# Kernel optimization log

Measured on AMD Instinct MI355X. Metric: run time of the kernel, lower is better.

The kernel has to match this reference:

```python
import jax, jax.numpy as jnp
import numpy as np


def _wn(v, g):
    # weight-norm: w[o, i] = g[o] * v[o, i] / ||v[o, :]||
    return g[:, None] * v / jnp.linalg.norm(v, axis=1, keepdims=True)


def setup_inputs() -> dict:
    key = jax.random.key(0)
    ks = jax.random.split(key, 8)
    B, C, H, W = 16, 512, 64, 64
    K, D = 2048, 64
    return {
        "z": jax.random.normal(ks[0], (B, C, H, W), dtype=jnp.float32),
        "codebook": jax.random.normal(ks[1], (K, D), dtype=jnp.float32),
        "in_v": jax.random.normal(ks[2], (D, C), dtype=jnp.float32),
        "in_g": jax.random.uniform(ks[3], (D,), dtype=jnp.float32, minval=0.5, maxval=1.5),
        "in_b": jax.random.normal(ks[4], (D,), dtype=jnp.float32) * 0.02,
        "out_v": jax.random.normal(ks[5], (C, D), dtype=jnp.float32),
        "out_g": jax.random.uniform(ks[6], (C,), dtype=jnp.float32, minval=0.5, maxval=1.5),
        "out_b": jax.random.normal(ks[7], (C,), dtype=jnp.float32) * 0.02,
    }


def reference(z, codebook, in_v, in_g, in_b, out_v, out_g, out_b):
    COMMIT_W = 0.25
    B, C, H, W = z.shape
    D = codebook.shape[1]

    Wi = _wn(in_v, in_g)    # [D, C]
    Wo = _wn(out_v, out_g)  # [C, D]

    # in_proj (1x1 conv): b c h w -> b d h w
    z_e = jnp.einsum('bchw,dc->bdhw', z, Wi) + in_b[None, :, None, None]

    # flatten tokens: (b h w) d
    z_e_flat = z_e.transpose(0, 2, 3, 1).reshape(-1, D)

    dist = (jnp.sum(z_e_flat * z_e_flat, axis=1, keepdims=True)
            - 2.0 * z_e_flat @ codebook.T
            + jnp.sum(codebook * codebook, axis=1)[None, :])
    indices_flat = jnp.argmin(dist, axis=1)            # [(BHW)]
    indices = indices_flat.reshape(B, H, W)

    z_q_flat = codebook[indices_flat]                  # gather [(BHW), D]
    z_q = z_q_flat.reshape(B, H, W, D).transpose(0, 3, 1, 2)  # b d h w

    sg = jax.lax.stop_gradient
    commitment_loss = jnp.mean((sg(z_e) - z_q) ** 2)
    codebook_loss = jnp.mean((sg(z_q) - z_e) ** 2)
    vq_loss = codebook_loss + COMMIT_W * commitment_loss

    # straight-through
    z_q_st = z_e + sg(z_q - z_e)

    # out_proj (1x1 conv): b d h w -> b c h w
    out = jnp.einsum('bdhw,cd->bchw', z_q_st, Wo) + out_b[None, :, None, None]
    return out, indices, vq_loss
```

## Files before the change

kernel.cpp:

```cpp
#include <hip/hip_runtime.h>
#include <math.h>

#define TOK_PER_BLK 128


__global__ void k_prep_wi(const float* __restrict__ v, const float* __restrict__ g,
                          float* __restrict__ wi){
  const int d = blockIdx.x;
  const int tid = threadIdx.x;
  float s = 0.f;
  for (int c = tid; c < 512; c += 256){ float x = v[d*512+c]; s = fmaf(x,x,s); }
  __shared__ float red[4];
  #pragma unroll
  for (int o = 32; o > 0; o >>= 1) s += __shfl_down(s, o);
  if ((tid & 63) == 0) red[tid >> 6] = s;
  __syncthreads();
  const float nrm = sqrtf(red[0]+red[1]+red[2]+red[3]);
  const float gd = g[d];
  for (int c = tid; c < 512; c += 256) wi[d*512+c] = gd * v[d*512+c] / nrm;
}

__global__ void k_prep_wo(const float* __restrict__ v, const float* __restrict__ g,
                          float* __restrict__ wot){
  const int c = blockIdx.x;
  const int d = threadIdx.x;
  const float x = v[c*64+d];
  float s = x*x;
  #pragma unroll
  for (int o = 32; o > 0; o >>= 1) s += __shfl_down(s, o);
  const float nrm = __shfl(sqrtf(s), 0);
  wot[d*512 + c] = g[c] * x / nrm;
}

__global__ void k_table(const float* __restrict__ cbk, const float* __restrict__ wot,
                        const float* __restrict__ ob, float* __restrict__ table,
                        float* __restrict__ ne){
  const int k = blockIdx.x;
  const int tid = threadIdx.x;
  __shared__ float e[64];
  if (tid < 64) e[tid] = cbk[k*64 + tid];
  __syncthreads();
  if (tid < 64){
    float x = e[tid];
    float s = x*x;
    #pragma unroll
    for (int o = 32; o > 0; o >>= 1) s += __shfl_down(s, o);
    if (tid == 0) ne[k] = s;
  }
  const int c = tid;
  float acc = ob[c];
  #pragma unroll 16
  for (int d = 0; d < 64; d++) acc = fmaf(e[d], wot[d*512 + c], acc);
  table[(size_t)k*512 + c] = acc;
}

__global__ __launch_bounds__(256, 2) void k_main(
    const float* __restrict__ z, const float* __restrict__ cbk,
    const float* __restrict__ wi, const float* __restrict__ inb,
    const float* __restrict__ ne, const float* __restrict__ table,
    float* __restrict__ out, float* __restrict__ oidx, double* __restrict__ loss)
{
  __shared__ __align__(16) float ze_s[64*132];
  __shared__ __align__(16) float sbuf[64*132];
  __shared__ int bidx_s[128];

  const int tid = threadIdx.x;
  const int t0  = blockIdx.x * TOK_PER_BLK;
  const int b   = t0 >> 12;
  const int hw0 = t0 & 4095;
  const float* zb = z + ((size_t)b << 21) + hw0;

  float* z_s  = sbuf;
  float* wi_s = sbuf + 32*132;
  float acc1[4][8];
  #pragma unroll
  for (int j = 0; j < 4; j++)
    #pragma unroll
    for (int i = 0; i < 8; i++) acc1[j][i] = 0.f;

  const int tt = tid & 31;
  const int dg = tid >> 5;

  for (int c0 = 0; c0 < 512; c0 += 32){
    {
      const int cc = tid >> 3, colb = (tid & 7) * 16;
      const float* src = zb + (size_t)(c0 + cc) * 4096 + colb;
      float* dst = &z_s[cc*132 + colb];
      #pragma unroll
      for (int j = 0; j < 4; j++)
        *(float4*)(dst + 4*j) = *(const float4*)(src + 4*j);
    }
    {
      #pragma unroll
      for (int j = 0; j < 8; j++){
        const int flat = tid + 256*j;
        const int d = flat >> 5, cc = flat & 31;
        wi_s[cc*68 + d] = wi[d*512 + c0 + cc];
      }
    }
    __syncthreads();
    #pragma unroll 4
    for (int cc = 0; cc < 32; cc++){
      const float4 zv = *(const float4*)&z_s[cc*132 + tt*4];
      const float4 wa = *(const float4*)&wi_s[cc*68 + dg*8];
      const float4 wb = *(const float4*)&wi_s[cc*68 + dg*8 + 4];
      const float zzv[4] = {zv.x, zv.y, zv.z, zv.w};
      const float wwv[8] = {wa.x, wa.y, wa.z, wa.w, wb.x, wb.y, wb.z, wb.w};
      #pragma unroll
      for (int j = 0; j < 4; j++)
        #pragma unroll
        for (int i = 0; i < 8; i++)
          acc1[j][i] = fmaf(zzv[j], wwv[i], acc1[j][i]);
    }
    __syncthreads();
  }
  #pragma unroll
  for (int i = 0; i < 8; i++){
    const int d = dg*8 + i;
    const float bd = inb[d];
    #pragma unroll
    for (int j = 0; j < 4; j++)
      ze_s[d*132 + tt*4 + j] = acc1[j][i] + bd;
  }
  __syncthreads();

  float* cb_s = sbuf;
  const int tg = tid & 15;
  const int kg = tid >> 4;
  float best[8]; int bidx[8];
  #pragma unroll
  for (int j = 0; j < 8; j++){ best[j] = INFINITY; bidx[j] = 0; }

  for (int kc = 0; kc < 2048; kc += 128){
    #pragma unroll
    for (int j = 0; j < 32; j++){
      const int flat = tid + 256*j;
      const int kk = flat >> 6, d = flat & 63;
      cb_s[d*132 + kk] = -2.0f * cbk[(size_t)(kc + kk)*64 + d];
    }
    __syncthreads();
    float acc[8][8];
    #pragma unroll
    for (int i = 0; i < 8; i++){
      const float nv = ne[kc + kg*8 + i];
      #pragma unroll
      for (int j = 0; j < 8; j++) acc[j][i] = nv;
    }
    #pragma unroll 4
    for (int d = 0; d < 64; d++){
      const float4 za  = *(const float4*)&ze_s[d*132 + tg*8];
      const float4 zb4 = *(const float4*)&ze_s[d*132 + tg*8 + 4];
      const float4 ca  = *(const float4*)&cb_s[d*132 + kg*8];
      const float4 cb4 = *(const float4*)&cb_s[d*132 + kg*8 + 4];
      const float zzv[8] = {za.x, za.y, za.z, za.w, zb4.x, zb4.y, zb4.z, zb4.w};
      const float ccv[8] = {ca.x, ca.y, ca.z, ca.w, cb4.x, cb4.y, cb4.z, cb4.w};
      #pragma unroll
      for (int j = 0; j < 8; j++)
        #pragma unroll
        for (int i = 0; i < 8; i++)
          acc[j][i] = fmaf(zzv[j], ccv[i], acc[j][i]);
    }
    #pragma unroll
    for (int i = 0; i < 8; i++){
      const int k = kc + kg*8 + i;
      #pragma unroll
      for (int j = 0; j < 8; j++)
        if (acc[j][i] < best[j]){ best[j] = acc[j][i]; bidx[j] = k; }
    }
    __syncthreads();
  }

  float* rb = sbuf;
  int*   ri = (int*)(sbuf + 2048);
  #pragma unroll
  for (int j = 0; j < 8; j++){
    const int t = tg*8 + j;
    rb[t*16 + kg] = best[j];
    ri[t*16 + kg] = bidx[j];
  }
  __syncthreads();

  float myloss = 0.f;
  if (tid < 128){
    const int t = tid;
    float bv = rb[t*16]; int bi = ri[t*16];
    #pragma unroll
    for (int q = 1; q < 16; q++){
      const float vq = rb[t*16 + q]; const int iq = ri[t*16 + q];
      if (vq < bv || (vq == bv && iq < bi)){ bv = vq; bi = iq; }
    }
    bidx_s[t] = bi;
    oidx[t0 + t] = (float)bi;
    const float* e = cbk + (size_t)bi * 64;
    #pragma unroll 8
    for (int d = 0; d < 64; d++){
      const float diff = ze_s[d*132 + t] - e[d];
      myloss = fmaf(diff, diff, myloss);
    }
  }
  #pragma unroll
  for (int o = 32; o > 0; o >>= 1) myloss += __shfl_down(myloss, o);
  if (tid < 128 && (tid & 63) == 0) atomicAdd(loss, (double)myloss);
  __syncthreads();

  {
    const int tl = tid & 127, cg = tid >> 7;
    const int myk = bidx_s[tl];
    const float* trow = table + ((size_t)myk << 9) + cg*256;
    float* ob = out + (((size_t)b) << 21) + hw0 + tl;
    #pragma unroll 4
    for (int ci = 0; ci < 64; ci++){
      const float4 v = *(const float4*)(trow + ci*4);
      const size_t cbase = (size_t)(cg*256 + ci*4) << 12;
      ob[cbase        ] = v.x;
      ob[cbase +  4096] = v.y;
      ob[cbase +  8192] = v.z;
      ob[cbase + 12288] = v.w;
    }
  }
}

__global__ void k_finish(const double* __restrict__ loss, float* __restrict__ oloss){
  *oloss = (float)(1.25 * (*loss) / 4194304.0);
}


extern "C" void kernel_launch(void* const* d_in, const int* in_sizes, int n_in,
                              void* d_out, int out_size, void* d_ws, size_t ws_size,
                              hipStream_t stream) {
  const float* z   = (const float*)d_in[0];
  const float* cbk = (const float*)d_in[1];
  const float* inv = (const float*)d_in[2];
  const float* ing = (const float*)d_in[3];
  const float* inb = (const float*)d_in[4];
  const float* ov  = (const float*)d_in[5];
  const float* og  = (const float*)d_in[6];
  const float* ob  = (const float*)d_in[7];

  float* ws    = (float*)d_ws;
  float* wi    = ws;
  float* wot   = ws + 32768;
  float* table = ws + 65536;
  float* ne    = ws + 65536 + 1048576;
  double* loss = (double*)(ws + 65536 + 1048576 + 2048);

  float* out   = (float*)d_out;
  float* oidx  = out + 33554432;
  float* oloss = out + 33619968;

  hipMemsetAsync(loss, 0, sizeof(double), stream);
  k_prep_wi<<<64, 256, 0, stream>>>(inv, ing, wi);
  k_prep_wo<<<512, 64, 0, stream>>>(ov, og, wot);
  k_table<<<2048, 512, 0, stream>>>(cbk, wot, ob, table, ne);
  k_main<<<512, 256, 0, stream>>>(z, cbk, wi, inb, ne, table, out, oidx, loss);
  k_finish<<<1, 1, 0, stream>>>(loss, oloss);
}
```

Before: 376.0 us.

## Split in-projection into separate kernel and retile codebook search with prefetch

Moves the 1x1 in-projection into its own kernel that computes 256 tokens per block with register-prefetched double buffering and a transposed Wi. It writes z_e to a workspace buffer. The VQ search kernel then reloads z_e and uses a larger 8x16 register tile, streaming the codebook in 256-entry, half-D chunks with register prefetch. This aims to raise arithmetic intensity and overlap loads, at the cost of an extra global round trip for z_e and an extra launch.

```diff
diff --git a/kernel.cpp b/kernel.cpp
--- a/kernel.cpp
+++ b/kernel.cpp
@@ -1,11 +1,10 @@
 #include <hip/hip_runtime.h>
 #include <math.h>
 
-#define TOK_PER_BLK 128
 
 
 __global__ void k_prep_wi(const float* __restrict__ v, const float* __restrict__ g,
-                          float* __restrict__ wi){
+                          float* __restrict__ wiT){
   const int d = blockIdx.x;
   const int tid = threadIdx.x;
   float s = 0.f;
@@ -17,7 +16,7 @@
   __syncthreads();
   const float nrm = sqrtf(red[0]+red[1]+red[2]+red[3]);
   const float gd = g[d];
-  for (int c = tid; c < 512; c += 256) wi[d*512+c] = gd * v[d*512+c] / nrm;
+  for (int c = tid; c < 512; c += 256) wiT[c*64 + d] = gd * v[d*512+c] / nrm;
 }
 
 __global__ void k_prep_wo(const float* __restrict__ v, const float* __restrict__ g,
@@ -54,127 +53,187 @@
   table[(size_t)k*512 + c] = acc;
 }
 
-__global__ __launch_bounds__(256, 2) void k_main(
-    const float* __restrict__ z, const float* __restrict__ cbk,
-    const float* __restrict__ wi, const float* __restrict__ inb,
+__global__ __launch_bounds__(256, 1) void k_inproj(
+    const float* __restrict__ z, const float* __restrict__ wiT,
+    const float* __restrict__ inb, float* __restrict__ ze)
+{
+  __shared__ __align__(16) float z_s[16*256];
+  __shared__ __align__(16) float wi_s[16*68];
+  const int tid = threadIdx.x;
+  const int T0  = blockIdx.x << 8;
+  const int b   = T0 >> 12;
+  const int hw0 = T0 & 4095;
+  const float* zb = z + ((size_t)b << 21) + hw0;
+
+  const int tgp = tid & 31;
+  const int dgp = tid >> 5;
+  const int ccb = tid >> 6;
+  const int c64 = tid & 63;
+
+  float acc[8][8];
+  #pragma unroll
+  for (int i = 0; i < 8; i++)
+    #pragma unroll
+    for (int j = 0; j < 8; j++) acc[i][j] = 0.f;
+
+  float4 pz[4]; float pw[4];
+  #pragma unroll
+  for (int q = 0; q < 4; q++){
+    pz[q] = *(const float4*)(zb + (size_t)(ccb + 4*q) * 4096 + c64*4);
+    pw[q] = wiT[(ccb + 4*q)*64 + c64];
+  }
+  #pragma unroll
+  for (int q = 0; q < 4; q++){
+    *(float4*)&z_s[(ccb + 4*q)*256 + c64*4] = pz[q];
+    wi_s[(ccb + 4*q)*68 + c64] = pw[q];
+  }
+  __syncthreads();
+
+  for (int c0 = 0;;){
+    const int nxt = c0 + 16;
+    if (nxt < 512){
+      #pragma unroll
+      for (int q = 0; q < 4; q++){
+        pz[q] = *(const float4*)(zb + (size_t)(nxt + ccb + 4*q) * 4096 + c64*4);
+        pw[q] = wiT[(nxt + ccb + 4*q)*64 + c64];
+      }
+    }
+    #pragma unroll 4
+    for (int cc = 0; cc < 16; cc++){
+      const float4 ta = *(const float4*)&z_s[cc*256 + tgp*4];
+      const float4 tb = *(const float4*)&z_s[cc*256 + 128 + tgp*4];
+      const float4 w0 = *(const float4*)&wi_s[cc*68 + dgp*8];
+      const float4 w1 = *(const float4*)&wi_s[cc*68 + dgp*8 + 4];
+      const float tv[8] = {ta.x,ta.y,ta.z,ta.w, tb.x,tb.y,tb.z,tb.w};
+      const float wv[8] = {w0.x,w0.y,w0.z,w0.w, w1.x,w1.y,w1.z,w1.w};
+      #pragma unroll
+      for (int i = 0; i < 8; i++)
+        #pragma unroll
+        for (int j = 0; j < 8; j++)
+          acc[i][j] = fmaf(tv[j], wv[i], acc[i][j]);
+    }
+    if (nxt >= 512) break;
+    __syncthreads();
+    #pragma unroll
+    for (int q = 0; q < 4; q++){
+      *(float4*)&z_s[(ccb + 4*q)*256 + c64*4] = pz[q];
+      wi_s[(ccb + 4*q)*68 + c64] = pw[q];
+    }
+    __syncthreads();
+    c0 = nxt;
+  }
+
+  #pragma unroll
+  for (int i = 0; i < 8; i++){
+    const int d = dgp*8 + i;
+    const float bd = inb[d];
+    float4 o0 = {acc[i][0]+bd, acc[i][1]+bd, acc[i][2]+bd, acc[i][3]+bd};
+    float4 o1 = {acc[i][4]+bd, acc[i][5]+bd, acc[i][6]+bd, acc[i][7]+bd};
+    *(float4*)(ze + (size_t)d*65536 + T0 + tgp*4)       = o0;
+    *(float4*)(ze + (size_t)d*65536 + T0 + 128 + tgp*4) = o1;
+  }
+}
+
+__global__ __launch_bounds__(256, 2) void k_main2(
+    const float* __restrict__ ze, const float* __restrict__ cbk,
     const float* __restrict__ ne, const float* __restrict__ table,
     float* __restrict__ out, float* __restrict__ oidx, double* __restrict__ loss)
 {
-  __shared__ __align__(16) float ze_s[64*132];
-  __shared__ __align__(16) float sbuf[64*132];
+  __shared__ __align__(16) float ze_s[64*128];
+  __shared__ __align__(16) float cb_s[32*260];
   __shared__ int bidx_s[128];
 
   const int tid = threadIdx.x;
-  const int t0  = blockIdx.x * TOK_PER_BLK;
+  const int t0  = blockIdx.x << 7;
   const int b   = t0 >> 12;
   const int hw0 = t0 & 4095;
-  const float* zb = z + ((size_t)b << 21) + hw0;
-
-  float* z_s  = sbuf;
-  float* wi_s = sbuf + 32*132;
-  float acc1[4][8];
-  #pragma unroll
-  for (int j = 0; j < 4; j++)
-    #pragma unroll
-    for (int i = 0; i < 8; i++) acc1[j][i] = 0.f;
-
-  const int tt = tid & 31;
-  const int dg = tid >> 5;
-
-  for (int c0 = 0; c0 < 512; c0 += 32){
-    {
-      const int cc = tid >> 3, colb = (tid & 7) * 16;
-      const float* src = zb + (size_t)(c0 + cc) * 4096 + colb;
-      float* dst = &z_s[cc*132 + colb];
-      #pragma unroll
-      for (int j = 0; j < 4; j++)
-        *(float4*)(dst + 4*j) = *(const float4*)(src + 4*j);
-    }
-    {
-      #pragma unroll
-      for (int j = 0; j < 8; j++){
-        const int flat = tid + 256*j;
-        const int d = flat >> 5, cc = flat & 31;
-        wi_s[cc*68 + d] = wi[d*512 + c0 + cc];
-      }
-    }
-    __syncthreads();
-    #pragma unroll 4
-    for (int cc = 0; cc < 32; cc++){
-      const float4 zv = *(const float4*)&z_s[cc*132 + tt*4];
-      const float4 wa = *(const float4*)&wi_s[cc*68 + dg*8];
-      const float4 wb = *(const float4*)&wi_s[cc*68 + dg*8 + 4];
-      const float zzv[4] = {zv.x, zv.y, zv.z, zv.w};
-      const float wwv[8] = {wa.x, wa.y, wa.z, wa.w, wb.x, wb.y, wb.z, wb.w};
-      #pragma unroll
-      for (int j = 0; j < 4; j++)
-        #pragma unroll
-        for (int i = 0; i < 8; i++)
-          acc1[j][i] = fmaf(zzv[j], wwv[i], acc1[j][i]);
-    }
-    __syncthreads();
-  }
-  #pragma unroll
-  for (int i = 0; i < 8; i++){
-    const int d = dg*8 + i;
-    const float bd = inb[d];
-    #pragma unroll
-    for (int j = 0; j < 4; j++)
-      ze_s[d*132 + tt*4 + j] = acc1[j][i] + bd;
-  }
-  __syncthreads();
-
-  float* cb_s = sbuf;
+
+  #pragma unroll
+  for (int j = 0; j < 8; j++){
+    const int idx = tid + 256*j;
+    const int row = idx >> 5, col4 = idx & 31;
+    *(float4*)&ze_s[row*128 + col4*4] =
+        *(const float4*)(ze + (size_t)row*65536 + t0 + col4*4);
+  }
+
   const int tg = tid & 15;
   const int kg = tid >> 4;
   float best[8]; int bidx[8];
   #pragma unroll
   for (int j = 0; j < 8; j++){ best[j] = INFINITY; bidx[j] = 0; }
 
-  for (int kc = 0; kc < 2048; kc += 128){
-    #pragma unroll
-    for (int j = 0; j < 32; j++){
-      const int flat = tid + 256*j;
-      const int kk = flat >> 6, d = flat & 63;
-      cb_s[d*132 + kk] = -2.0f * cbk[(size_t)(kc + kk)*64 + d];
-    }
+  float acc[8][16];
+  float4 pv[8];
+  {
+    const float* src = cbk + (size_t)tid * 64;
+    #pragma unroll
+    for (int q = 0; q < 8; q++) pv[q] = *(const float4*)(src + q*4);
+  }
+
+  for (int s = 0; s < 16; s++){
     __syncthreads();
-    float acc[8][8];
-    #pragma unroll
-    for (int i = 0; i < 8; i++){
-      const float nv = ne[kc + kg*8 + i];
-      #pragma unroll
-      for (int j = 0; j < 8; j++) acc[j][i] = nv;
-    }
+    #pragma unroll
+    for (int q = 0; q < 8; q++){
+      const float* p = (const float*)&pv[q];
+      #pragma unroll
+      for (int r = 0; r < 4; r++) cb_s[(q*4+r)*260 + tid] = -2.0f * p[r];
+    }
+    if (s < 15){
+      const int s1 = s + 1;
+      const float* src = cbk + (size_t)(((s1 >> 1) << 8) + tid) * 64 + (s1 & 1)*32;
+      #pragma unroll
+      for (int q = 0; q < 8; q++) pv[q] = *(const float4*)(src + q*4);
+    }
+    __syncthreads();
+
+    const int dh = s & 1, kc = (s >> 1) << 8;
+    if (dh == 0){
+      #pragma unroll
+      for (int q = 0; q < 4; q++){
+        const float4 nv = *(const float4*)&ne[kc + kg*16 + q*4];
+        const float nn[4] = {nv.x, nv.y, nv.z, nv.w};
+        #pragma unroll
+        for (int r = 0; r < 4; r++)
+          #pragma unroll
+          for (int j = 0; j < 8; j++) acc[j][q*4+r] = nn[r];
+      }
+    }
+    const int dbase = dh << 5;
     #pragma unroll 4
-    for (int d = 0; d < 64; d++){
-      const float4 za  = *(const float4*)&ze_s[d*132 + tg*8];
-      const float4 zb4 = *(const float4*)&ze_s[d*132 + tg*8 + 4];
-      const float4 ca  = *(const float4*)&cb_s[d*132 + kg*8];
-      const float4 cb4 = *(const float4*)&cb_s[d*132 + kg*8 + 4];
-      const float zzv[8] = {za.x, za.y, za.z, za.w, zb4.x, zb4.y, zb4.z, zb4.w};
-      const float ccv[8] = {ca.x, ca.y, ca.z, ca.w, cb4.x, cb4.y, cb4.z, cb4.w};
+    for (int d = 0; d < 32; d++){
+      const int dr = dbase + d;
+      const float4 za = *(const float4*)&ze_s[dr*128 + tg*4];
+      const float4 zb = *(const float4*)&ze_s[dr*128 + 64 + tg*4];
+      const float4 c0 = *(const float4*)&cb_s[d*260 + kg*16];
+      const float4 c1 = *(const float4*)&cb_s[d*260 + kg*16 + 4];
+      const float4 c2 = *(const float4*)&cb_s[d*260 + kg*16 + 8];
+      const float4 c3 = *(const float4*)&cb_s[d*260 + kg*16 + 12];
+      const float zz[8]  = {za.x,za.y,za.z,za.w, zb.x,zb.y,zb.z,zb.w};
+      const float cv[16] = {c0.x,c0.y,c0.z,c0.w, c1.x,c1.y,c1.z,c1.w,
+                            c2.x,c2.y,c2.z,c2.w, c3.x,c3.y,c3.z,c3.w};
       #pragma unroll
       for (int j = 0; j < 8; j++)
         #pragma unroll
-        for (int i = 0; i < 8; i++)
-          acc[j][i] = fmaf(zzv[j], ccv[i], acc[j][i]);
-    }
-    #pragma unroll
-    for (int i = 0; i < 8; i++){
-      const int k = kc + kg*8 + i;
-      #pragma unroll
-      for (int j = 0; j < 8; j++)
-        if (acc[j][i] < best[j]){ best[j] = acc[j][i]; bidx[j] = k; }
-    }
-    __syncthreads();
-  }
-
-  float* rb = sbuf;
-  int*   ri = (int*)(sbuf + 2048);
+        for (int i = 0; i < 16; i++)
+          acc[j][i] = fmaf(zz[j], cv[i], acc[j][i]);
+    }
+    if (dh == 1){
+      #pragma unroll
+      for (int i = 0; i < 16; i++){
+        const int k = kc + kg*16 + i;
+        #pragma unroll
+        for (int j = 0; j < 8; j++)
+          if (acc[j][i] < best[j]){ best[j] = acc[j][i]; bidx[j] = k; }
+      }
+    }
+  }
+  __syncthreads();
+
+  float* rb = cb_s;
+  int*   ri = (int*)(cb_s + 2048);
   #pragma unroll
   for (int j = 0; j < 8; j++){
-    const int t = tg*8 + j;
+    const int t = (j < 4) ? (tg*4 + j) : (64 + tg*4 + (j - 4));
     rb[t*16 + kg] = best[j];
     ri[t*16 + kg] = bidx[j];
   }
@@ -194,7 +253,7 @@
     const float* e = cbk + (size_t)bi * 64;
     #pragma unroll 8
     for (int d = 0; d < 64; d++){
-      const float diff = ze_s[d*132 + t] - e[d];
+      const float diff = ze_s[d*128 + t] - e[d];
       myloss = fmaf(diff, diff, myloss);
     }
   }
@@ -238,20 +297,22 @@
   const float* ob  = (const float*)d_in[7];
 
   float* ws    = (float*)d_ws;
-  float* wi    = ws;
+  float* wiT   = ws;
   float* wot   = ws + 32768;
   float* table = ws + 65536;
   float* ne    = ws + 65536 + 1048576;
-  double* loss = (double*)(ws + 65536 + 1048576 + 2048);
+  double* loss = (double*)(ws + 1116160);
+  float* zebuf = ws + 2097152;
 
   float* out   = (float*)d_out;
   float* oidx  = out + 33554432;
   float* oloss = out + 33619968;
 
   hipMemsetAsync(loss, 0, sizeof(double), stream);
-  k_prep_wi<<<64, 256, 0, stream>>>(inv, ing, wi);
+  k_prep_wi<<<64, 256, 0, stream>>>(inv, ing, wiT);
   k_prep_wo<<<512, 64, 0, stream>>>(ov, og, wot);
   k_table<<<2048, 512, 0, stream>>>(cbk, wot, ob, table, ne);
-  k_main<<<512, 256, 0, stream>>>(z, cbk, wi, inb, ne, table, out, oidx, loss);
+  k_inproj<<<256, 256, 0, stream>>>(z, wiT, inb, zebuf);
+  k_main2<<<512, 256, 0, stream>>>(zebuf, cbk, ne, table, out, oidx, loss);
   k_finish<<<1, 1, 0, stream>>>(loss, oloss);
 }
```

Result: faster. 340.1 us (-9.5%).
